# Kernel optimization log

Hardware: AMD Instinct MI355X
Metric: run time of the kernel (lower is better)

Reference implementation:

```python
import jax, jax.numpy as jnp
import numpy as np
from jax import lax

B, N, C = 16, 2304, 768
H_HEADS, D = 12, 64  # num_heads, head_dim
SCALE = 9.0 ** (-0.5)  # equivalent_head_dim ** -0.5


def setup_inputs() -> dict:
    key = jax.random.key(0)
    ks = jax.random.split(key, 8)
    return {
        "x": jax.random.normal(ks[0], (B, N, C), dtype=jnp.float32),
        "qkv_w": jax.random.normal(ks[1], (3 * C + 3 * D, C), dtype=jnp.float32) * 0.02,
        "qkv_b": jax.random.normal(ks[2], (3 * C + 3 * D,), dtype=jnp.float32) * 0.02,
        "w1": jax.random.normal(ks[3], (1, H_HEADS, D, D), dtype=jnp.float32) * 0.02,
        "w2": jax.random.normal(ks[4], (1, H_HEADS, D, D), dtype=jnp.float32) * 0.02,
        "w3": jax.random.normal(ks[5], (D, 1, 3, 3), dtype=jnp.float32) * 0.02,
        "proj_w": jax.random.normal(ks[6], (C, C + D), dtype=jnp.float32) * 0.02,
        "proj_b": jax.random.normal(ks[7], (C,), dtype=jnp.float32) * 0.02,
        "h": 48,
        "w": 48,
    }


def _inner_swiglu(k, v, w1, w2, lr=1.0):
    # k, v: [B, H, N, d]; w1, w2: [1, H, d, d]
    z1 = jnp.einsum('bhnd,hde->bhne', k, w1[0])
    z2 = jnp.einsum('bhnd,hde->bhne', k, w2[0])
    sig = jax.nn.sigmoid(z2)
    a = z2 * sig
    e = -v / float(v.shape[2]) * SCALE
    g1 = jnp.einsum('bhnd,bhne->bhde', k, e * a)
    g2 = jnp.einsum('bhnd,bhne->bhde', k, e * z1 * (sig * (1.0 + z2 * (1.0 - sig))))
    g1 = g1 / (jnp.linalg.norm(g1, axis=-2, keepdims=True) + 1.0)
    g2 = g2 / (jnp.linalg.norm(g2, axis=-2, keepdims=True) + 1.0)
    return w1 - lr * g1, w2 - lr * g2  # [B, H, d, d]


def _inner_3x3dwc(k, v, w3, hh, ww, lr=1.0):
    # k, v: [B, d, h, w]; w3: [d, 1, 3, 3]
    b, c = k.shape[0], k.shape[1]
    e = -v / float(hh * ww) * SCALE
    kp = jnp.pad(k, ((0, 0), (0, 0), (1, 1), (1, 1)))
    dots = []
    for ys in (0, 1, 2):  # 1 + dy
        for xs in (0, 1, 2):  # 1 + dx
            dots.append(jnp.sum(kp[:, :, ys:ys + hh, xs:xs + ww] * e, axis=(-2, -1)))
    g = jnp.stack(dots, axis=-1).reshape(b * c, 1, 3, 3)
    g = g / (jnp.sqrt(jnp.sum(g * g, axis=(-2, -1), keepdims=True)) + 1.0)
    return jnp.tile(w3, (b, 1, 1, 1)) - lr * g  # [B*d, 1, 3, 3]


def reference(x, qkv_w, qkv_b, w1, w2, w3, proj_w, proj_b, h, w):
    b, n, c = x.shape
    nh = w1.shape[1]
    d = c // nh
    qkv = x @ qkv_w.T + qkv_b  # [B, N, 3C + 3d]
    q1, k1, v1, q2, k2, v2 = jnp.split(
        qkv, [c, 2 * c, 3 * c, 3 * c + d, 3 * c + 2 * d], axis=-1)
    heads = lambda t: t.reshape(b, n, nh, d).transpose(0, 2, 1, 3)
    q1, k1, v1 = heads(q1), heads(k1), heads(v1)

    w1u, w2u = _inner_swiglu(k1, v1, w1, w2)
    x1 = jnp.einsum('bhnd,bhde->bhne', q1, w1u) * jax.nn.silu(
        jnp.einsum('bhnd,bhde->bhne', q1, w2u))
    x1 = x1.transpose(0, 2, 1, 3).reshape(b, n, c)

    spatial = lambda t: t.reshape(b, h, w, d).transpose(0, 3, 1, 2)  # [B, d, h, w]
    q2s, k2s, v2s = spatial(q2), spatial(k2), spatial(v2)
    w3u = _inner_3x3dwc(k2s, v2s, w3, h, w)
    x2 = lax.conv_general_dilated(
        q2s.reshape(1, b * d, h, w), w3u,
        window_strides=(1, 1), padding=((1, 1), (1, 1)),
        feature_group_count=b * d,
        dimension_numbers=('NCHW', 'OIHW', 'NCHW'))
    x2 = x2.reshape(b, d, n).transpose(0, 2, 1)  # [B, N, d]

    out = jnp.concatenate([x1, x2], axis=-1) @ proj_w.T + proj_b
    return out
```

## Files before the change

### kernel.cpp

```cpp
#include <hip/hip_runtime.h>
#include <hip/hip_bf16.h>
#include <math.h>

#define B_   16
#define N_   2304
#define C_   768
#define H_   12
#define D_   64
#define M_   (B_*N_)
#define NQKV 2496
#define NPAD 2560
#define CCP  832
#define EVS  (-1.0f/6912.0f)

typedef __bf16 bf16x8 __attribute__((ext_vector_type(8)));
typedef __bf16 bf16x4 __attribute__((ext_vector_type(4)));
typedef float  f32x4  __attribute__((ext_vector_type(4)));

static __device__ __forceinline__ void gload_lds16(const void* g, void* l) {
  __builtin_amdgcn_global_load_lds((const __attribute__((address_space(1))) void*)g,
                                   (__attribute__((address_space(3))) void*)l, 16, 0, 0);
}

static __device__ __forceinline__ bf16x8 ld8(const __bf16* p) {
  bf16x4 lo = *(const bf16x4*)p;
  bf16x4 hi = *(const bf16x4*)(p + 4);
  return __builtin_shufflevector(lo, hi, 0,1,2,3,4,5,6,7);
}

__global__ __launch_bounds__(256) void cvt_all(
    const float* __restrict__ x, const float* __restrict__ qkv_w,
    const float* __restrict__ qkv_b, const float* __restrict__ proj_w,
    __bf16* __restrict__ xb, __bf16* __restrict__ wqkvb,
    float* __restrict__ qkvbp, __bf16* __restrict__ pwb)
{
  const int blk = blockIdx.x;
  if (blk < 13824) {
    int i = blk * 256 + threadIdx.x;
    const float4* p = (const float4*)(x + (size_t)i * 8);
    float4 a = p[0], b = p[1];
    bf16x8 o = {(__bf16)a.x,(__bf16)a.y,(__bf16)a.z,(__bf16)a.w,
                (__bf16)b.x,(__bf16)b.y,(__bf16)b.z,(__bf16)b.w};
    *(bf16x8*)(xb + (size_t)i * 8) = o;
  } else if (blk < 14784) {
    int i = (blk - 13824) * 256 + threadIdx.x;
    int n = i / 96, c8 = i - n * 96;
    bf16x8 o;
    if (n < NQKV) {
      const float4* p = (const float4*)(qkv_w + (size_t)n * 768 + c8 * 8);
      float4 a = p[0], b = p[1];
      o = (bf16x8){(__bf16)a.x,(__bf16)a.y,(__bf16)a.z,(__bf16)a.w,
                   (__bf16)b.x,(__bf16)b.y,(__bf16)b.z,(__bf16)b.w};
    } else {
      o = (bf16x8){(__bf16)0.f,(__bf16)0.f,(__bf16)0.f,(__bf16)0.f,
                   (__bf16)0.f,(__bf16)0.f,(__bf16)0.f,(__bf16)0.f};
    }
    *(bf16x8*)(wqkvb + (size_t)n * 768 + c8 * 8) = o;
    if (i < NPAD) qkvbp[i] = (i < NQKV) ? qkv_b[i] : 0.0f;
  } else {
    int i = (blk - 14784) * 256 + threadIdx.x;
    if (i >= 79872) return;
    const float4* p = (const float4*)(proj_w + (size_t)i * 8);
    float4 a = p[0], b = p[1];
    bf16x8 o = {(__bf16)a.x,(__bf16)a.y,(__bf16)a.z,(__bf16)a.w,
                (__bf16)b.x,(__bf16)b.y,(__bf16)b.z,(__bf16)b.w};
    *(bf16x8*)(pwb + (size_t)i * 8) = o;
  }
}

template<int OUTF32>
__global__ __launch_bounds__(512, 2) void gemm8(
    const __bf16* __restrict__ A, const __bf16* __restrict__ Bt,
    const float* __restrict__ bias, void* __restrict__ Cout,
    const int K, const int ldc, const int nbn, const int KT)
{
  __shared__ __align__(16) __bf16 sA[2][2][128 * 64];
  __shared__ __align__(16) __bf16 sB[2][2][128 * 64];
  const int tid  = threadIdx.x;
  const int lane = tid & 63;
  const int wid  = tid >> 6;
  const int wm = wid >> 2;
  const int wn = wid & 3;
  const int l15 = lane & 15, lq = lane >> 4;

  const int nwg = gridDim.x;
  const int swz = ((int)blockIdx.x & 7) * (nwg >> 3) + ((int)blockIdx.x >> 3);
  const int bm = swz / nbn;
  const int bn = swz - bm * nbn;

  const int strow = tid >> 3;
  const int stoff = strow * 64 + (tid & 7) * 8;
  const __bf16* gA = A  + (size_t)((size_t)bm * 256 + strow) * K + ((tid & 7) ^ (strow & 7)) * 8;
  const __bf16* gB = Bt + (size_t)((size_t)bn * 256 + strow) * K + ((tid & 7) ^ (strow & 7)) * 8;

  f32x4 acc[2][4][2][2];
  #pragma unroll
  for (int a = 0; a < 2; ++a)
    #pragma unroll
    for (int m = 0; m < 4; ++m)
      #pragma unroll
      for (int b = 0; b < 2; ++b)
        #pragma unroll
        for (int n = 0; n < 2; ++n) acc[a][m][b][n] = (f32x4){0.f,0.f,0.f,0.f};

  bf16x8 af0[4][2], af1[4][2], bf0[2][2], bf1[2][2];

#define STAGE_A(q, h, T) do {                                                   \
    const size_t ko_ = (size_t)(T) * 64;                                        \
    gload_lds16(gA + (size_t)((h)*128 +  0) * K + ko_, &sA[q][h][stoff]);       \
    gload_lds16(gA + (size_t)((h)*128 + 64) * K + ko_, &sA[q][h][4096 + stoff]);\
  } while (0)
#define STAGE_B(q, h, T) do {                                                   \
    const size_t ko_ = (size_t)(T) * 64;                                        \
    gload_lds16(gB + (size_t)((h)*128 +  0) * K + ko_, &sB[q][h][stoff]);       \
    gload_lds16(gB + (size_t)((h)*128 + 64) * K + ko_, &sB[q][h][4096 + stoff]);\
  } while (0)
#define LOADA(DST, h, q) do {                                                   \
    _Pragma("unroll") for (int mf_ = 0; mf_ < 4; ++mf_) {                       \
      const int r_ = wm * 64 + mf_ * 16 + l15;                                  \
      _Pragma("unroll") for (int kk_ = 0; kk_ < 2; ++kk_)                       \
        DST[mf_][kk_] = *(const bf16x8*)&sA[q][h][r_ * 64 + (((kk_*4+lq) ^ (r_&7)) * 8)]; \
    } } while (0)
#define LOADB(DST, h, q) do {                                                   \
    _Pragma("unroll") for (int nf_ = 0; nf_ < 2; ++nf_) {                       \
      const int c_ = wn * 32 + nf_ * 16 + l15;                                  \
      _Pragma("unroll") for (int kk_ = 0; kk_ < 2; ++kk_)                       \
        DST[nf_][kk_] = *(const bf16x8*)&sB[q][h][c_ * 64 + (((kk_*4+lq) ^ (c_&7)) * 8)]; \
    } } while (0)
#define MMA(a_, b_, AF, BF) do {                                                \
    __builtin_amdgcn_s_setprio(1);                                              \
    _Pragma("unroll") for (int kk_ = 0; kk_ < 2; ++kk_)                         \
    _Pragma("unroll") for (int mf_ = 0; mf_ < 4; ++mf_)                         \
    _Pragma("unroll") for (int nf_ = 0; nf_ < 2; ++nf_)                         \
      acc[a_][mf_][b_][nf_] = __builtin_amdgcn_mfma_f32_16x16x32_bf16(          \
          AF[mf_][kk_], BF[nf_][kk_], acc[a_][mf_][b_][nf_], 0, 0, 0);          \
    __builtin_amdgcn_s_setprio(0);                                              \
  } while (0)
#define BAR  __builtin_amdgcn_s_barrier()
#define LGKM do { asm volatile("s_waitcnt lgkmcnt(0)" ::: "memory");            \
                  __builtin_amdgcn_sched_barrier(0); } while (0)
#define VMW4 asm volatile("s_waitcnt vmcnt(4)" ::: "memory")
#define VMW0 asm volatile("s_waitcnt vmcnt(0)" ::: "memory")

  STAGE_A(0, 0, 0); STAGE_A(0, 1, 0); STAGE_B(0, 0, 0); STAGE_B(0, 1, 0);
  STAGE_B(1, 0, 1);
  STAGE_A(1, 1, 1);
  VMW4;
  BAR;

  for (int t = 0; t + 1 < KT; t += 2) {
    LOADA(af0, 0, 0); LOADB(bf0, 0, 0);
    STAGE_A(1, 0, t + 1); STAGE_B(1, 1, t + 1);
    BAR; LGKM; MMA(0, 0, af0, bf0); BAR;
    LOADA(af1, 1, 0);
    BAR; LGKM; MMA(1, 0, af1, bf0); BAR;
    LOADB(bf1, 1, 0);
    if (t + 2 < KT) STAGE_B(0, 0, t + 2);
    BAR; LGKM; MMA(1, 1, af1, bf1); BAR;
    if (t + 2 < KT) STAGE_A(0, 1, t + 2);
    BAR; MMA(0, 1, af0, bf1);
    if (t + 2 < KT) { VMW4; } else { VMW0; }
    BAR;
    LOADA(af0, 0, 1); LOADB(bf0, 0, 1);
    if (t + 2 < KT) { STAGE_A(0, 0, t + 2); STAGE_B(0, 1, t + 2); }
    BAR; LGKM; MMA(0, 0, af0, bf0); BAR;
    LOADA(af1, 1, 1);
    BAR; LGKM; MMA(1, 0, af1, bf0); BAR;
    LOADB(bf1, 1, 1);
    if (t + 3 < KT) STAGE_B(1, 0, t + 3);
    BAR; LGKM; MMA(1, 1, af1, bf1); BAR;
    if (t + 3 < KT) STAGE_A(1, 1, t + 3);
    BAR; MMA(0, 1, af0, bf1);
    if (t + 3 < KT) { VMW4; } else { VMW0; }
    BAR;
  }
  if (KT & 1) {
    LOADA(af0, 0, 0); LOADB(bf0, 0, 0);
    MMA(0, 0, af0, bf0);
    LOADA(af1, 1, 0);
    MMA(1, 0, af1, bf0);
    LOADB(bf1, 1, 0);
    MMA(1, 1, af1, bf1);
    MMA(0, 1, af0, bf1);
  }
#undef STAGE_A
#undef STAGE_B
#undef LOADA
#undef LOADB
#undef MMA

  #pragma unroll
  for (int b = 0; b < 2; ++b)
    #pragma unroll
    for (int nf = 0; nf < 2; ++nf) {
      const int col = bn * 256 + b * 128 + wn * 32 + nf * 16 + l15;
      const float bs = bias[col];
      #pragma unroll
      for (int a = 0; a < 2; ++a)
        #pragma unroll
        for (int mf = 0; mf < 4; ++mf) {
          const int row0 = bm * 256 + a * 128 + wm * 64 + mf * 16 + lq * 4;
          #pragma unroll
          for (int r = 0; r < 4; ++r) {
            float v = acc[a][mf][b][nf][r] + bs;
            if (OUTF32) ((float*)Cout)[(size_t)(row0 + r) * ldc + col] = v;
            else        ((__bf16*)Cout)[(size_t)(row0 + r) * ldc + col] = (__bf16)v;
          }
        }
    }
}

__global__ __launch_bounds__(256, 3) void inner_grad(
    const __bf16* __restrict__ qkv, const float* __restrict__ w1,
    const float* __restrict__ w2, float* __restrict__ gpart)
{
  const int blk = blockIdx.x;
  const int bh = blk >> 2, seg = blk & 3;
  const int b = bh / H_, h = bh - b * H_;
  const int tid = threadIdx.x, wid = tid >> 6, lane = tid & 63;
  const int wr = wid >> 1, wc = wid & 1, l15 = lane & 15, lq = lane >> 4;

  __shared__ __bf16 w1T[64 * 72], w2T[64 * 72];
  __shared__ __bf16 kNt1[64 * 72];
  __shared__ __bf16 kT[64 * 72], t2T[64 * 72];

  const float* w1p = w1 + h * 4096;
  const float* w2p = w2 + h * 4096;
  for (int idx = tid; idx < 4096; idx += 256) {
    int d = idx >> 6, e = idx & 63;
    w1T[e * 72 + d] = (__bf16)w1p[idx];
    w2T[e * 72 + d] = (__bf16)w2p[idx];
  }

  f32x4 g1a[2][2], g2a[2][2];
  #pragma unroll
  for (int i = 0; i < 2; ++i)
    #pragma unroll
    for (int j = 0; j < 2; ++j) { g1a[i][j] = (f32x4){0.f,0.f,0.f,0.f}; g2a[i][j] = (f32x4){0.f,0.f,0.f,0.f}; }

  const size_t rowb = (size_t)b * N_;
  const int koff = C_ + h * D_;
  const int voff = 2 * C_ + h * D_;
  const int sn = tid >> 2, sdb = tid & 3;
  __syncthreads();

  for (int ci = 0; ci < 9; ++ci) {
    const int n0 = seg * 576 + ci * 64;
    {
      const __bf16* src = qkv + (rowb + n0 + sn) * (size_t)NPAD + koff + sdb * 16;
      bf16x8 va = *(const bf16x8*)src;
      bf16x8 vb = *(const bf16x8*)(src + 8);
      __bf16* kn = &kNt1[sn * 72 + sdb * 16];
      *(bf16x4*)(kn + 0)  = __builtin_shufflevector(va, va, 0,1,2,3);
      *(bf16x4*)(kn + 4)  = __builtin_shufflevector(va, va, 4,5,6,7);
      *(bf16x4*)(kn + 8)  = __builtin_shufflevector(vb, vb, 0,1,2,3);
      *(bf16x4*)(kn + 12) = __builtin_shufflevector(vb, vb, 4,5,6,7);
      #pragma unroll
      for (int j = 0; j < 8; ++j) kT[(sdb * 16 + j) * 72 + sn] = va[j];
      #pragma unroll
      for (int j = 0; j < 8; ++j) kT[(sdb * 16 + 8 + j) * 72 + sn] = vb[j];
    }
    __syncthreads();

    f32x4 z1[2][2], z2[2][2];
    #pragma unroll
    for (int i = 0; i < 2; ++i)
      #pragma unroll
      for (int j = 0; j < 2; ++j) { z1[i][j] = (f32x4){0.f,0.f,0.f,0.f}; z2[i][j] = (f32x4){0.f,0.f,0.f,0.f}; }
    #pragma unroll
    for (int kk = 0; kk < 2; ++kk) {
      bf16x8 af[2], b1[2], b2[2];
      #pragma unroll
      for (int mi = 0; mi < 2; ++mi)
        af[mi] = ld8(&kNt1[(wr * 32 + mi * 16 + l15) * 72 + kk * 32 + lq * 8]);
      #pragma unroll
      for (int ni = 0; ni < 2; ++ni) {
        int e = wc * 32 + ni * 16 + l15;
        b1[ni] = ld8(&w1T[e * 72 + kk * 32 + lq * 8]);
        b2[ni] = ld8(&w2T[e * 72 + kk * 32 + lq * 8]);
      }
      #pragma unroll
      for (int mi = 0; mi < 2; ++mi)
        #pragma unroll
        for (int ni = 0; ni < 2; ++ni) {
          z1[mi][ni] = __builtin_amdgcn_mfma_f32_16x16x32_bf16(af[mi], b1[ni], z1[mi][ni], 0, 0, 0);
          z2[mi][ni] = __builtin_amdgcn_mfma_f32_16x16x32_bf16(af[mi], b2[ni], z2[mi][ni], 0, 0, 0);
        }
    }
    __syncthreads();

    #pragma unroll
    for (int mi = 0; mi < 2; ++mi)
      #pragma unroll
      for (int ni = 0; ni < 2; ++ni) {
        int nl = wr * 32 + mi * 16 + lq * 4;
        int e  = wc * 32 + ni * 16 + l15;
        const __bf16* vp = qkv + (rowb + n0 + nl) * (size_t)NPAD + voff + e;
        #pragma unroll
        for (int r = 0; r < 4; ++r) {
          float vv  = (float)vp[(size_t)r * NPAD];
          float ev  = vv * EVS;
          float z1v = z1[mi][ni][r], z2v = z2[mi][ni][r];
          float sg  = 1.0f / (1.0f + __expf(-z2v));
          float t1  = ev * (z2v * sg);
          float t2  = ev * z1v * (sg * (1.0f + z2v * (1.0f - sg)));
          kNt1[e * 72 + nl + r] = (__bf16)t1;
          t2T [e * 72 + nl + r] = (__bf16)t2;
        }
      }
    __syncthreads();

    #pragma unroll
    for (int kk = 0; kk < 2; ++kk) {
      bf16x8 af[2], b1[2], b2[2];
      #pragma unroll
      for (int mi = 0; mi < 2; ++mi)
        af[mi] = ld8(&kT[(wr * 32 + mi * 16 + l15) * 72 + kk * 32 + lq * 8]);
      #pragma unroll
      for (int ni = 0; ni < 2; ++ni) {
        int e = wc * 32 + ni * 16 + l15;
        b1[ni] = ld8(&kNt1[e * 72 + kk * 32 + lq * 8]);
        b2[ni] = ld8(&t2T [e * 72 + kk * 32 + lq * 8]);
      }
      #pragma unroll
      for (int mi = 0; mi < 2; ++mi)
        #pragma unroll
        for (int ni = 0; ni < 2; ++ni) {
          g1a[mi][ni] = __builtin_amdgcn_mfma_f32_16x16x32_bf16(af[mi], b1[ni], g1a[mi][ni], 0, 0, 0);
          g2a[mi][ni] = __builtin_amdgcn_mfma_f32_16x16x32_bf16(af[mi], b2[ni], g2a[mi][ni], 0, 0, 0);
        }
    }
    __syncthreads();
  }

  float* gp = gpart + (size_t)blk * 8192;
  #pragma unroll
  for (int mi = 0; mi < 2; ++mi)
    #pragma unroll
    for (int ni = 0; ni < 2; ++ni)
      #pragma unroll
      for (int r = 0; r < 4; ++r) {
        int d = wr * 32 + mi * 16 + lq * 4 + r;
        int e = wc * 32 + ni * 16 + l15;
        gp[d * 64 + e]        = g1a[mi][ni][r];
        gp[4096 + d * 64 + e] = g2a[mi][ni][r];
      }
}

__global__ __launch_bounds__(256) void inner_upd(
    const float* __restrict__ gpart, const float* __restrict__ w1,
    const float* __restrict__ w2, __bf16* __restrict__ wu)
{
  const int bh = blockIdx.x;
  const int h = bh % H_;
  const int tid = threadIdx.x;
  __shared__ float g1[64 * 65], g2[64 * 65];
  __shared__ float nrm1[64], nrm2[64];
  const float* w1p = w1 + h * 4096;
  const float* w2p = w2 + h * 4096;

  for (int idx = tid; idx < 4096; idx += 256) {
    float s1 = 0.f, s2 = 0.f;
    #pragma unroll
    for (int s = 0; s < 4; ++s) {
      const float* gp = gpart + (size_t)(bh * 4 + s) * 8192;
      s1 += gp[idx]; s2 += gp[4096 + idx];
    }
    int d = idx >> 6, e = idx & 63;
    g1[d * 65 + e] = s1; g2[d * 65 + e] = s2;
  }
  __syncthreads();
  if (tid < 128) {
    const float* gs = (tid < 64) ? g1 : g2;
    int e = tid & 63;
    float s = 0.f;
    for (int d = 0; d < 64; ++d) { float gv = gs[d * 65 + e]; s += gv * gv; }
    float rn = 1.0f / (sqrtf(s) + 1.0f);
    if (tid < 64) nrm1[e] = rn; else nrm2[e] = rn;
  }
  __syncthreads();
  __bf16* wub = wu + (size_t)bh * 8192;
  for (int idx = tid; idx < 4096; idx += 256) {
    int d = idx >> 6, e = idx & 63;
    wub[idx]        = (__bf16)(w1p[idx] - g1[d * 65 + e] * nrm1[e]);
    wub[4096 + idx] = (__bf16)(w2p[idx] - g2[d * 65 + e] * nrm2[e]);
  }
}

__global__ __launch_bounds__(256) void inner_apply(
    const __bf16* __restrict__ qkv, const __bf16* __restrict__ wu,
    __bf16* __restrict__ concat)
{
  const int blk = blockIdx.x;
  const int bh = blk / 6, seg = blk - bh * 6;
  const int b = bh / H_, h = bh - b * H_;
  const int tid = threadIdx.x, wid = tid >> 6, lane = tid & 63;
  const int wr = wid >> 1, wc = wid & 1, l15 = lane & 15, lq = lane >> 4;

  __shared__ __bf16 w1T[64 * 72], w2T[64 * 72], qN[64 * 72];
  const __bf16* wub = wu + (size_t)bh * 8192;
  for (int idx = tid; idx < 4096; idx += 256) {
    int d = idx >> 6, e = idx & 63;
    w1T[e * 72 + d] = wub[idx];
    w2T[e * 72 + d] = wub[4096 + idx];
  }

  const size_t rowb = (size_t)b * N_;
  const int qoff = h * D_;
  const int sn = tid >> 2, sdb = tid & 3;

  for (int ci = 0; ci < 6; ++ci) {
    const int n0 = seg * 384 + ci * 64;
    {
      const __bf16* src = qkv + (rowb + n0 + sn) * (size_t)NPAD + qoff + sdb * 16;
      bf16x8 va = *(const bf16x8*)src;
      bf16x8 vb = *(const bf16x8*)(src + 8);
      __bf16* kn = &qN[sn * 72 + sdb * 16];
      *(bf16x4*)(kn + 0)  = __builtin_shufflevector(va, va, 0,1,2,3);
      *(bf16x4*)(kn + 4)  = __builtin_shufflevector(va, va, 4,5,6,7);
      *(bf16x4*)(kn + 8)  = __builtin_shufflevector(vb, vb, 0,1,2,3);
      *(bf16x4*)(kn + 12) = __builtin_shufflevector(vb, vb, 4,5,6,7);
    }
    __syncthreads();
    f32x4 y1[2][2], y2[2][2];
    #pragma unroll
    for (int i = 0; i < 2; ++i)
      #pragma unroll
      for (int j = 0; j < 2; ++j) { y1[i][j] = (f32x4){0.f,0.f,0.f,0.f}; y2[i][j] = (f32x4){0.f,0.f,0.f,0.f}; }
    #pragma unroll
    for (int kk = 0; kk < 2; ++kk) {
      bf16x8 af[2], b1[2], b2[2];
      #pragma unroll
      for (int mi = 0; mi < 2; ++mi)
        af[mi] = ld8(&qN[(wr * 32 + mi * 16 + l15) * 72 + kk * 32 + lq * 8]);
      #pragma unroll
      for (int ni = 0; ni < 2; ++ni) {
        int e = wc * 32 + ni * 16 + l15;
        b1[ni] = ld8(&w1T[e * 72 + kk * 32 + lq * 8]);
        b2[ni] = ld8(&w2T[e * 72 + kk * 32 + lq * 8]);
      }
      #pragma unroll
      for (int mi = 0; mi < 2; ++mi)
        #pragma unroll
        for (int ni = 0; ni < 2; ++ni) {
          y1[mi][ni] = __builtin_amdgcn_mfma_f32_16x16x32_bf16(af[mi], b1[ni], y1[mi][ni], 0, 0, 0);
          y2[mi][ni] = __builtin_amdgcn_mfma_f32_16x16x32_bf16(af[mi], b2[ni], y2[mi][ni], 0, 0, 0);
        }
    }
    #pragma unroll
    for (int mi = 0; mi < 2; ++mi)
      #pragma unroll
      for (int ni = 0; ni < 2; ++ni) {
        int nl = wr * 32 + mi * 16 + lq * 4;
        int e  = wc * 32 + ni * 16 + l15;
        #pragma unroll
        for (int r = 0; r < 4; ++r) {
          float a1 = y1[mi][ni][r], a2 = y2[mi][ni][r];
          float sg = 1.0f / (1.0f + __expf(-a2));
          concat[(rowb + n0 + nl + r) * (size_t)CCP + h * D_ + e] = (__bf16)(a1 * (a2 * sg));
        }
      }
    __syncthreads();
  }
}

__global__ __launch_bounds__(256) void dwc_grad2(const __bf16* __restrict__ qkv,
                                                 float* __restrict__ w3p) {
  const int blk = blockIdx.x;
  const int b = blk / 12, sp = blk - b * 12;
  const int tid = threadIdx.x, dd = tid & 63, rl = tid >> 6;
  __shared__ __bf16 kS[6 * 50 * 64];
  __shared__ float red[4][9][64];
  for (int i = tid; i < 9600; i += 256) ((unsigned*)kS)[i] = 0u;
  __syncthreads();
  const size_t base = (size_t)b * N_ * NPAD;
  for (int i = tid; i < 6 * 48 * 8; i += 256) {
    int y6 = i / 384; int rem = i - y6 * 384; int x = rem >> 3; int c8 = rem & 7;
    int y = 4 * sp - 1 + y6;
    if (y >= 0 && y < 48) {
      int p = y * 48 + x;
      bf16x8 v = *(const bf16x8*)&qkv[base + (size_t)p * NPAD + 2368 + c8 * 8];
      *(bf16x8*)&kS[((y6 * 50) + x + 1) * 64 + c8 * 8] = v;
    }
  }
  __syncthreads();
  float acc[9];
  #pragma unroll
  for (int j = 0; j < 9; ++j) acc[j] = 0.f;
  const int y = 4 * sp + rl;
  for (int x = 0; x < 48; ++x) {
    int p = y * 48 + x;
    float e = (float)qkv[base + (size_t)p * NPAD + 2432 + dd] * EVS;
    #pragma unroll
    for (int j = 0; j < 9; ++j) {
      int ys = j / 3, xs = j - ys * 3;
      acc[j] += (float)kS[((rl + ys) * 50 + x + xs) * 64 + dd] * e;
    }
  }
  #pragma unroll
  for (int j = 0; j < 9; ++j) red[rl][j][dd] = acc[j];
  __syncthreads();
  if (rl == 0) {
    #pragma unroll
    for (int j = 0; j < 9; ++j) {
      float s = red[0][j][dd] + red[1][j][dd] + red[2][j][dd] + red[3][j][dd];
      w3p[((size_t)(b * 12 + sp) * 64 + dd) * 9 + j] = s;
    }
  }
}

__global__ __launch_bounds__(256) void dwc_upd(const float* __restrict__ w3p,
    const float* __restrict__ w3, float* __restrict__ w3u) {
  int i = blockIdx.x * 256 + threadIdx.x;
  if (i >= 1024) return;
  int b = i >> 6, dd = i & 63;
  float g[9];
  #pragma unroll
  for (int j = 0; j < 9; ++j) g[j] = 0.f;
  for (int sp = 0; sp < 12; ++sp)
    #pragma unroll
    for (int j = 0; j < 9; ++j)
      g[j] += w3p[((size_t)(b * 12 + sp) * 64 + dd) * 9 + j];
  float ss = 0.f;
  #pragma unroll
  for (int j = 0; j < 9; ++j) ss += g[j] * g[j];
  float rn = 1.0f / (sqrtf(ss) + 1.0f);
  #pragma unroll
  for (int j = 0; j < 9; ++j) w3u[i * 9 + j] = w3[dd * 9 + j] - g[j] * rn;
}

__global__ __launch_bounds__(256) void dwc_apply2(const __bf16* __restrict__ qkv,
    const float* __restrict__ w3u, __bf16* __restrict__ concat) {
  const int blk = blockIdx.x;
  const int b = blk / 12, sp = blk - b * 12;
  const int tid = threadIdx.x, dd = tid & 63, rl = tid >> 6;
  __shared__ __bf16 qS[6 * 50 * 64];
  for (int i = tid; i < 9600; i += 256) ((unsigned*)qS)[i] = 0u;
  __syncthreads();
  const size_t base = (size_t)b * N_ * NPAD;
  for (int i = tid; i < 6 * 48 * 8; i += 256) {
    int y6 = i / 384; int rem = i - y6 * 384; int x = rem >> 3; int c8 = rem & 7;
    int y = 4 * sp - 1 + y6;
    if (y >= 0 && y < 48) {
      int p = y * 48 + x;
      bf16x8 v = *(const bf16x8*)&qkv[base + (size_t)p * NPAD + 2304 + c8 * 8];
      *(bf16x8*)&qS[((y6 * 50) + x + 1) * 64 + c8 * 8] = v;
    }
  }
  __syncthreads();
  float wv[9];
  #pragma unroll
  for (int j = 0; j < 9; ++j) wv[j] = w3u[(size_t)(b * 64 + dd) * 9 + j];
  const int y = 4 * sp + rl;
  for (int x = 0; x < 48; ++x) {
    float s = 0.f;
    #pragma unroll
    for (int j = 0; j < 9; ++j) {
      int ys = j / 3, xs = j - ys * 3;
      s += (float)qS[((rl + ys) * 50 + x + xs) * 64 + dd] * wv[j];
    }
    int p = y * 48 + x;
    concat[((size_t)b * N_ + p) * CCP + 768 + dd] = (__bf16)s;
  }
}

extern "C" void kernel_launch(void* const* d_in, const int* in_sizes, int n_in,
                              void* d_out, int out_size, void* d_ws, size_t ws_size,
                              hipStream_t stream) {
  const float* x      = (const float*)d_in[0];
  const float* qkv_w  = (const float*)d_in[1];
  const float* qkv_b  = (const float*)d_in[2];
  const float* w1     = (const float*)d_in[3];
  const float* w2     = (const float*)d_in[4];
  const float* w3     = (const float*)d_in[5];
  const float* proj_w = (const float*)d_in[6];
  const float* proj_b = (const float*)d_in[7];

  char* ws = (char*)d_ws;
  __bf16* xb     = (__bf16*)ws;
  __bf16* wqkvb  = (__bf16*)(ws + 56623104);
  float*  qkvbp  = (float*) (ws + 60555264);
  __bf16* concat = (__bf16*)ws;
  __bf16* qkvb16 = (__bf16*)(ws + 66060288);
  __bf16* pwb    = (__bf16*)(ws + 254803968);
  float*  w3u    = (float*) (ws + 256180224);
  float*  w3p    = (float*) (ws + 256217088);
  float*  gpart  = (float*) (ws + 256659456);
  __bf16* wu     = (__bf16*)(ws + 281825280);

  cvt_all<<<15096, 256, 0, stream>>>(x, qkv_w, qkv_b, proj_w, xb, wqkvb, qkvbp, pwb);

  gemm8<0><<<1440, 512, 0, stream>>>(xb, wqkvb, qkvbp, (void*)qkvb16,
                                     768, NPAD, 10, 12);

  inner_grad <<< 768, 256, 0, stream>>>(qkvb16, w1, w2, gpart);
  inner_upd  <<< 192, 256, 0, stream>>>(gpart, w1, w2, wu);
  inner_apply<<<1152, 256, 0, stream>>>(qkvb16, wu, concat);
  dwc_grad2 <<<192, 256, 0, stream>>>(qkvb16, w3p);
  dwc_upd   <<<  4, 256, 0, stream>>>(w3p, w3, w3u);
  dwc_apply2<<<192, 256, 0, stream>>>(qkvb16, w3u, concat);

  gemm8<1><<<432, 512, 0, stream>>>(concat, pwb, proj_b, d_out,
                                    832, 768, 3, 13);
}
```

Measured before the change: 434.0 us.

## Replace 8-phase interleaved GEMM pipeline with simple double-buffered K loop

Replaces the hand-interleaved eight-phase schedule in the bf16 GEMM, which staged half-tiles between MFMA groups under many barriers, with a plain double buffer over the K tile. Each iteration prefetches the next full 256x64 A and B tiles into the other LDS buffer, computes the four MFMA quadrants, then waits on vmcnt(0) and one barrier. This cuts barrier and waitcnt overhead and simplifies the code. In exchange it loses the fine-grained overlap of LDS reads and global loads with MFMA, and the full vmcnt(0) wait may expose memory latency.

```diff
diff --git a/kernel.cpp b/kernel.cpp
--- a/kernel.cpp
+++ b/kernel.cpp
@@ -69,13 +69,13 @@
 }
 
 template<int OUTF32>
-__global__ __launch_bounds__(512, 2) void gemm8(
+__global__ __launch_bounds__(512, 2) void gemmW(
     const __bf16* __restrict__ A, const __bf16* __restrict__ Bt,
     const float* __restrict__ bias, void* __restrict__ Cout,
     const int K, const int ldc, const int nbn, const int KT)
 {
-  __shared__ __align__(16) __bf16 sA[2][2][128 * 64];
-  __shared__ __align__(16) __bf16 sB[2][2][128 * 64];
+  __shared__ __align__(16) __bf16 sA[2][256 * 64];
+  __shared__ __align__(16) __bf16 sB[2][256 * 64];
   const int tid  = threadIdx.x;
   const int lane = tid & 63;
   const int wid  = tid >> 6;
@@ -105,27 +105,24 @@
 
   bf16x8 af0[4][2], af1[4][2], bf0[2][2], bf1[2][2];
 
-#define STAGE_A(q, h, T) do {                                                   \
+#define STAGE(q, T) do {                                                        \
     const size_t ko_ = (size_t)(T) * 64;                                        \
-    gload_lds16(gA + (size_t)((h)*128 +  0) * K + ko_, &sA[q][h][stoff]);       \
-    gload_lds16(gA + (size_t)((h)*128 + 64) * K + ko_, &sA[q][h][4096 + stoff]);\
-  } while (0)
-#define STAGE_B(q, h, T) do {                                                   \
-    const size_t ko_ = (size_t)(T) * 64;                                        \
-    gload_lds16(gB + (size_t)((h)*128 +  0) * K + ko_, &sB[q][h][stoff]);       \
-    gload_lds16(gB + (size_t)((h)*128 + 64) * K + ko_, &sB[q][h][4096 + stoff]);\
-  } while (0)
+    _Pragma("unroll")                                                           \
+    for (int j_ = 0; j_ < 4; ++j_) {                                            \
+      gload_lds16(gA + (size_t)(j_ * 64) * K + ko_, &sA[q][j_ * 4096 + stoff]); \
+      gload_lds16(gB + (size_t)(j_ * 64) * K + ko_, &sB[q][j_ * 4096 + stoff]); \
+    } } while (0)
 #define LOADA(DST, h, q) do {                                                   \
     _Pragma("unroll") for (int mf_ = 0; mf_ < 4; ++mf_) {                       \
-      const int r_ = wm * 64 + mf_ * 16 + l15;                                  \
+      const int r_ = (h) * 128 + wm * 64 + mf_ * 16 + l15;                      \
       _Pragma("unroll") for (int kk_ = 0; kk_ < 2; ++kk_)                       \
-        DST[mf_][kk_] = *(const bf16x8*)&sA[q][h][r_ * 64 + (((kk_*4+lq) ^ (r_&7)) * 8)]; \
+        DST[mf_][kk_] = *(const bf16x8*)&sA[q][r_ * 64 + (((kk_*4+lq) ^ (r_&7)) * 8)]; \
     } } while (0)
 #define LOADB(DST, h, q) do {                                                   \
     _Pragma("unroll") for (int nf_ = 0; nf_ < 2; ++nf_) {                       \
-      const int c_ = wn * 32 + nf_ * 16 + l15;                                  \
+      const int c_ = (h) * 128 + wn * 32 + nf_ * 16 + l15;                      \
       _Pragma("unroll") for (int kk_ = 0; kk_ < 2; ++kk_)                       \
-        DST[nf_][kk_] = *(const bf16x8*)&sB[q][h][c_ * 64 + (((kk_*4+lq) ^ (c_&7)) * 8)]; \
+        DST[nf_][kk_] = *(const bf16x8*)&sB[q][c_ * 64 + (((kk_*4+lq) ^ (c_&7)) * 8)]; \
     } } while (0)
 #define MMA(a_, b_, AF, BF) do {                                                \
     __builtin_amdgcn_s_setprio(1);                                              \
@@ -136,55 +133,27 @@
           AF[mf_][kk_], BF[nf_][kk_], acc[a_][mf_][b_][nf_], 0, 0, 0);          \
     __builtin_amdgcn_s_setprio(0);                                              \
   } while (0)
-#define BAR  __builtin_amdgcn_s_barrier()
-#define LGKM do { asm volatile("s_waitcnt lgkmcnt(0)" ::: "memory");            \
-                  __builtin_amdgcn_sched_barrier(0); } while (0)
-#define VMW4 asm volatile("s_waitcnt vmcnt(4)" ::: "memory")
-#define VMW0 asm volatile("s_waitcnt vmcnt(0)" ::: "memory")
-
-  STAGE_A(0, 0, 0); STAGE_A(0, 1, 0); STAGE_B(0, 0, 0); STAGE_B(0, 1, 0);
-  STAGE_B(1, 0, 1);
-  STAGE_A(1, 1, 1);
-  VMW4;
-  BAR;
-
-  for (int t = 0; t + 1 < KT; t += 2) {
-    LOADA(af0, 0, 0); LOADB(bf0, 0, 0);
-    STAGE_A(1, 0, t + 1); STAGE_B(1, 1, t + 1);
-    BAR; LGKM; MMA(0, 0, af0, bf0); BAR;
-    LOADA(af1, 1, 0);
-    BAR; LGKM; MMA(1, 0, af1, bf0); BAR;
-    LOADB(bf1, 1, 0);
-    if (t + 2 < KT) STAGE_B(0, 0, t + 2);
-    BAR; LGKM; MMA(1, 1, af1, bf1); BAR;
-    if (t + 2 < KT) STAGE_A(0, 1, t + 2);
-    BAR; MMA(0, 1, af0, bf1);
-    if (t + 2 < KT) { VMW4; } else { VMW0; }
-    BAR;
-    LOADA(af0, 0, 1); LOADB(bf0, 0, 1);
-    if (t + 2 < KT) { STAGE_A(0, 0, t + 2); STAGE_B(0, 1, t + 2); }
-    BAR; LGKM; MMA(0, 0, af0, bf0); BAR;
-    LOADA(af1, 1, 1);
-    BAR; LGKM; MMA(1, 0, af1, bf0); BAR;
-    LOADB(bf1, 1, 1);
-    if (t + 3 < KT) STAGE_B(1, 0, t + 3);
-    BAR; LGKM; MMA(1, 1, af1, bf1); BAR;
-    if (t + 3 < KT) STAGE_A(1, 1, t + 3);
-    BAR; MMA(0, 1, af0, bf1);
-    if (t + 3 < KT) { VMW4; } else { VMW0; }
-    BAR;
-  }
-  if (KT & 1) {
-    LOADA(af0, 0, 0); LOADB(bf0, 0, 0);
-    MMA(0, 0, af0, bf0);
-    LOADA(af1, 1, 0);
-    MMA(1, 0, af1, bf0);
-    LOADB(bf1, 1, 0);
-    MMA(1, 1, af1, bf1);
-    MMA(0, 1, af0, bf1);
-  }
-#undef STAGE_A
-#undef STAGE_B
+
+  STAGE(0, 0);
+  asm volatile("s_waitcnt vmcnt(0)" ::: "memory");
+  __builtin_amdgcn_s_barrier();
+
+  for (int t = 0; t < KT; ++t) {
+    const int q = t & 1;
+    if (t + 1 < KT) STAGE(q ^ 1, t + 1);
+
+    LOADB(bf0, 0, q); LOADB(bf1, 1, q);
+    LOADA(af0, 0, q);
+    MMA(0, 0, af0, bf0); MMA(0, 1, af0, bf1);
+    LOADA(af1, 1, q);
+    MMA(1, 0, af1, bf0); MMA(1, 1, af1, bf1);
+
+    if (t + 1 < KT) {
+      asm volatile("s_waitcnt vmcnt(0)" ::: "memory");
+      __builtin_amdgcn_s_barrier();
+    }
+  }
+#undef STAGE
 #undef LOADA
 #undef LOADB
 #undef MMA
@@ -590,7 +559,7 @@
 
   cvt_all<<<15096, 256, 0, stream>>>(x, qkv_w, qkv_b, proj_w, xb, wqkvb, qkvbp, pwb);
 
-  gemm8<0><<<1440, 512, 0, stream>>>(xb, wqkvb, qkvbp, (void*)qkvb16,
+  gemmW<0><<<1440, 512, 0, stream>>>(xb, wqkvb, qkvbp, (void*)qkvb16,
                                      768, NPAD, 10, 12);
 
   inner_grad <<< 768, 256, 0, stream>>>(qkvb16, w1, w2, gpart);
@@ -600,6 +569,6 @@
   dwc_upd   <<<  4, 256, 0, stream>>>(w3p, w3, w3u);
   dwc_apply2<<<192, 256, 0, stream>>>(qkvb16, w3u, concat);
 
-  gemm8<1><<<432, 512, 0, stream>>>(concat, pwb, proj_b, d_out,
+  gemmW<1><<<432, 512, 0, stream>>>(concat, pwb, proj_b, d_out,
                                     832, 768, 3, 13);
 }
```

Result: no change. 440.3 us (+1.4%).
